# Kernel tuning notes

Measured on AMD Instinct MI355X. Metric: run time of the kernel, lower is better.

The kernel has to match this reference:

```python
import jax, jax.numpy as jnp
import numpy as np

B, L, D = 4, 2048, 1024
MD = D // 4      # memory_dim = dim // 4
K = 5            # kernel_size
DIL = 1          # dilation
EPS = 1e-6


def rmsnorm(x, w):
    return w * x * jax.lax.rsqrt(jnp.mean(x * x, axis=-1, keepdims=True) + EPS)


def setup_inputs() -> dict:
    key = jax.random.key(0)
    ks = jax.random.split(key, 16)
    n = lambda k, shape, s=0.02: jax.random.normal(k, shape, jnp.float32) * s
    return dict(
        x=jax.random.normal(ks[0], (B, L, D), jnp.float32),
        memory_state=jnp.zeros((B, MD), jnp.float32),
        norm_w=jnp.ones((D,), jnp.float32),
        dw_kernel=n(ks[1], (D, 1, K), 0.1),   # depthwise conv [O,I/g,K]
        dw_bias=jnp.zeros((D,), jnp.float32),
        pw_kernel=n(ks[2], (D, D)),           # 1x1 conv as [out,in]
        pw_bias=jnp.zeros((D,), jnp.float32),
        Win_w=n(ks[3], (MD, D)), Win_b=jnp.zeros((MD,), jnp.float32),
        Wf_w=n(ks[4], (MD, D + MD)), Wf_b=jnp.ones((MD,), jnp.float32),  # forget bias init 1.0
        Wu_w=n(ks[5], (MD, D + MD)), Wu_b=jnp.zeros((MD,), jnp.float32),
        Wo_w=n(ks[6], (D, D + MD)), Wo_b=jnp.zeros((D,), jnp.float32),
        router_w=n(ks[7], (2, D)), router_b=jnp.zeros((2,), jnp.float32),
        e0_w1=n(ks[8], (D, D)), e0_b1=jnp.zeros((D,), jnp.float32),
        e0_w2=n(ks[9], (D, D)), e0_b2=jnp.zeros((D,), jnp.float32),
        e1_w1=n(ks[10], (D, D)), e1_b1=jnp.zeros((D,), jnp.float32),
        e1_w2=n(ks[11], (D, D)), e1_b2=jnp.zeros((D,), jnp.float32),
        fnorm_w=jnp.ones((D,), jnp.float32),
        down_w=n(ks[12], (D // 4, D)), down_b=jnp.zeros((D // 4,), jnp.float32),
        up_w=n(ks[13], (D, D // 4)), up_b=jnp.zeros((D,), jnp.float32),
    )


def reference(x, memory_state, norm_w, dw_kernel, dw_bias, pw_kernel, pw_bias,
              Win_w, Win_b, Wf_w, Wf_b, Wu_w, Wu_b, Wo_w, Wo_b,
              router_w, router_b, e0_w1, e0_b1, e0_w2, e0_b2,
              e1_w1, e1_b1, e1_w2, e1_b2, fnorm_w, down_w, down_b, up_w, up_b):
    resid = x
    xn = rmsnorm(x, norm_w)                              # [B,L,D]

    # --- causal depthwise conv (left pad (K-1)*DIL == torch pad-both + slice[:L]) + pointwise ---
    P = (K - 1) * DIL
    xc = jnp.swapaxes(xn, 1, 2)                          # [B,D,L]
    xc = jax.lax.conv_general_dilated(
        xc, dw_kernel, window_strides=(1,), padding=[(P, 0)],
        rhs_dilation=(DIL,), dimension_numbers=('NCH', 'OIH', 'NCH'),
        feature_group_count=D) + dw_bias[None, :, None]
    x_conv = jnp.einsum('bdl,ed->ble', xc, pw_kernel) + pw_bias  # [B,L,D]

    # --- structured state recurrence (gated, scan over time) ---
    Wf_x, Wf_m = Wf_w[:, :D], Wf_w[:, D:]
    Wu_x, Wu_m = Wu_w[:, :D], Wu_w[:, D:]
    Wo_x, Wo_m = Wo_w[:, :D], Wo_w[:, D:]
    # precompute all x-dependent projections: [L,B,*]
    fx = jnp.einsum('bld,md->lbm', xn, Wf_x) + Wf_b
    ux = jnp.einsum('bld,md->lbm', xn, Wu_x) + Wu_b
    ox = jnp.einsum('bld,ed->lbe', xn, Wo_x) + Wo_b
    xm = jax.nn.silu(jnp.einsum('bld,md->lbm', xn, Win_w) + Win_b)
    xt = jnp.swapaxes(xn, 0, 1)                          # [L,B,D]

    def step(m, inp):
        fx_t, ux_t, ox_t, xm_t, x_t = inp
        f = jax.nn.sigmoid(fx_t + m @ Wf_m.T)
        u = jax.nn.sigmoid(ux_t + m @ Wu_m.T)
        m2 = f * m + u * xm_t
        out = x_t + ox_t + m2 @ Wo_m.T
        return m2, out

    new_mem, rec = jax.lax.scan(step, memory_state, (fx, ux, ox, xm, xt))
    x_rec = jnp.swapaxes(rec, 0, 1)                      # [B,L,D]

    y = x_conv + x_rec

    # --- enhanced gated fusion (2-expert soft MoE) ---
    r = jax.nn.softmax(y @ router_w.T + router_b, axis=-1)   # [B,L,2]
    e0 = jax.nn.silu(y @ e0_w1.T + e0_b1) @ e0_w2.T + e0_b2
    e1 = jax.nn.silu(y @ e1_w1.T + e1_b1) @ e1_w2.T + e1_b2
    y = rmsnorm(y + r[..., 0:1] * e0 + r[..., 1:2] * e1, fnorm_w)

    # --- low-rank FF (exact GELU) + residual ---
    ff = jax.nn.gelu(y @ down_w.T + down_b, approximate=False) @ up_w.T + up_b
    out = y + ff + resid
    return out, new_mem
```

## Files before the change

### kernel.cpp

```cpp
#include <hip/hip_runtime.h>
#include <hip/hip_bf16.h>

#define DD 1024
#define MDD 256
#define LL 2048
#define BB 4
#define NROWS (BB*LL)

typedef short bf16x8 __attribute__((ext_vector_type(8)));
typedef float f32x4 __attribute__((ext_vector_type(4)));
typedef int   i32x4 __attribute__((ext_vector_type(4)));

__device__ __forceinline__ short f2b(float x){
  __hip_bfloat16 h = __float2bfloat16(x);
  return *reinterpret_cast<short*>(&h);
}
__device__ __forceinline__ float b2f(short s){
  return __uint_as_float(((unsigned)(unsigned short)s) << 16);
}
__device__ __forceinline__ float frcp(float x){
#if __has_builtin(__builtin_amdgcn_rcpf)
  return __builtin_amdgcn_rcpf(x);
#else
  float r; asm("v_rcp_f32 %0, %1" : "=v"(r) : "v"(x)); return r;
#endif
}
__device__ __forceinline__ float fsigmoid(float x){
  return frcp(1.f + __expf(-x));
}
__device__ __forceinline__ float sel4(f32x4 a, int kg){
  float lo = (kg & 1) ? a[1] : a[0];
  float hi = (kg & 1) ? a[3] : a[2];
  return (kg & 2) ? hi : lo;
}

struct CvtDesc {
  const float* src; const float* src2; short* dstb; float* dstf;
  int n, cols, sld, soff, dld, mode;
};
struct CvtArgs { CvtDesc d[20]; };

__global__ __launch_bounds__(256) void cvt_all(CvtArgs a){
  int di = blockIdx.x >> 6;
  CvtDesc d = a.d[di];
  int base = (blockIdx.x & 63)*256 + threadIdx.x;
  for (int i = base; i < d.n; i += 64*256){
    int r = i / d.cols, c = i - r*d.cols;
    float v = d.src[(size_t)r*d.sld + d.soff + c];
    if (d.mode == 2) v += d.src2[i];
    if (d.mode == 0) d.dstb[(size_t)r*d.dld + c] = f2b(v);
    else             d.dstf[i] = v;
  }
}

__global__ __launch_bounds__(256) void rmsnorm_k(const float* __restrict__ x,
                                                 const float* __restrict__ w,
                                                 short* __restrict__ xn){
  int row = blockIdx.x, tid = threadIdx.x;
  const float* xr = x + (size_t)row*DD;
  float4 v = *(const float4*)&xr[tid*4];
  float ss = v.x*v.x + v.y*v.y + v.z*v.z + v.w*v.w;
  __shared__ float red[256];
  red[tid] = ss; __syncthreads();
  for (int s = 128; s > 0; s >>= 1){ if (tid < s) red[tid] += red[tid+s]; __syncthreads(); }
  float scale = rsqrtf(red[0]/(float)DD + 1e-6f);
  const float* wr = w + tid*4;
  short4 o;
  o.x = f2b(v.x*wr[0]*scale); o.y = f2b(v.y*wr[1]*scale);
  o.z = f2b(v.z*wr[2]*scale); o.w = f2b(v.w*wr[3]*scale);
  *(short4*)&xn[(size_t)row*2048 + tid*4] = o;
}

__global__ __launch_bounds__(256) void dwconv_k(const short* __restrict__ xnA,
                                                const float* __restrict__ dwk,
                                                const float* __restrict__ dwb,
                                                short* __restrict__ xcA){
  size_t i = (size_t)blockIdx.x*256 + threadIdx.x;
  int d = (int)(i & (DD-1));
  int l = (int)((i >> 10) & (LL-1));
  int b = (int)(i >> 21);
  float acc = dwb[d];
  const float* kk = dwk + d*5;
  #pragma unroll
  for (int k = 0; k < 5; ++k){
    int ll = l + k - 4;
    if (ll >= 0) acc += b2f(xnA[((size_t)(b*LL + ll))*2048 + d]) * kk[k];
  }
  xcA[((size_t)(b*LL + l))*2048 + 1024 + d] = f2b(acc);
}

template<int ACT, int OUTMODE, int PERMUTE, int DUAL>
__global__ __launch_bounds__(256) void gemm_bt(
    const short* __restrict__ A, const short* __restrict__ Bw,
    const float* __restrict__ bias, const float* __restrict__ add0,
    const float* __restrict__ add1, void* __restrict__ Cout, short* __restrict__ Cout2,
    const short* A_b, const short* Bw_b, const float* bias_b, void* Cout_b,
    int M, int N, int K, int lda, int ldb, int nbn, int nsplit){
  __shared__ __align__(16) short As[128*32];
  __shared__ __align__(16) short Bs[128*32];
  int bid = (int)blockIdx.x;
  bid = (bid & 7)*((int)gridDim.x >> 3) + (bid >> 3);
  if (DUAL && bid >= nsplit){
    A = A_b; Bw = Bw_b; bias = bias_b; Cout = Cout_b; bid -= nsplit;
  }
  int bm = bid / nbn, bn = bid % nbn;
  int tid = threadIdx.x, lane = tid & 63, w = tid >> 6;
  int wm = (w >> 1)*64, wn = (w & 1)*64;
  const int r0 = lane & 15, kg = lane >> 4;

  f32x4 acc[4][4];
  #pragma unroll
  for (int i = 0; i < 4; ++i)
    #pragma unroll
    for (int j = 0; j < 4; ++j)
      #pragma unroll
      for (int r = 0; r < 4; ++r) acc[i][j][r] = 0.f;

  const int c0 = w*64 + lane;
  const int c1 = c0 + 256;
  const short* a0 = &A [(size_t)(bm*128 + (c0 >> 2))*lda + (c0 & 3)*8];
  const short* a1 = &A [(size_t)(bm*128 + (c1 >> 2))*lda + (c1 & 3)*8];
  const short* b0 = &Bw[(size_t)(bn*128 + (c0 >> 2))*ldb + (c0 & 3)*8];
  const short* b1 = &Bw[(size_t)(bn*128 + (c1 >> 2))*ldb + (c1 & 3)*8];

  for (int k0 = 0; k0 < K; k0 += 32){
    __builtin_amdgcn_global_load_lds((const __attribute__((address_space(1))) void*)(a0 + k0),
                                     (__attribute__((address_space(3))) void*)&As[w*512], 16, 0, 0);
    __builtin_amdgcn_global_load_lds((const __attribute__((address_space(1))) void*)(b0 + k0),
                                     (__attribute__((address_space(3))) void*)&Bs[w*512], 16, 0, 0);
    __builtin_amdgcn_global_load_lds((const __attribute__((address_space(1))) void*)(a1 + k0),
                                     (__attribute__((address_space(3))) void*)&As[2048 + w*512], 16, 0, 0);
    __builtin_amdgcn_global_load_lds((const __attribute__((address_space(1))) void*)(b1 + k0),
                                     (__attribute__((address_space(3))) void*)&Bs[2048 + w*512], 16, 0, 0);
    __syncthreads();
    bf16x8 av[4], bv[4];
    #pragma unroll
    for (int i = 0; i < 4; ++i) av[i] = *(const bf16x8*)&As[(wm + i*16 + r0)*32 + kg*8];
    #pragma unroll
    for (int j = 0; j < 4; ++j) bv[j] = *(const bf16x8*)&Bs[(wn + j*16 + r0)*32 + kg*8];
    #pragma unroll
    for (int i = 0; i < 4; ++i)
      #pragma unroll
      for (int j = 0; j < 4; ++j)
        acc[i][j] = __builtin_amdgcn_mfma_f32_16x16x32_bf16(av[i], bv[j], acc[i][j], 0, 0, 0);
    __syncthreads();
  }

  #pragma unroll
  for (int i = 0; i < 4; ++i){
    int grb = bm*128 + wm + i*16 + kg*4;
    #pragma unroll
    for (int j = 0; j < 4; ++j){
      int gc = bn*128 + wn + j*16 + r0;
      float bvv = bias ? bias[gc] : 0.f;
      #pragma unroll
      for (int r = 0; r < 4; ++r){
        int gr = grb + r;
        float v = acc[i][j][r] + bvv;
        if (ACT == 1) v = v / (1.f + __expf(-v));
        else if (ACT == 2) v = 0.5f*v*(1.f + erff(v*0.70710678118f));
        size_t orow = PERMUTE ? (size_t)((gr & 3)*LL + (gr >> 2)) : (size_t)gr;
        size_t oi = orow*(size_t)N + gc;
        if (add0) v += add0[oi];
        if (add1) v += add1[oi];
        if (OUTMODE == 0) ((float*)Cout)[oi] = v;
        else if (OUTMODE == 1) ((float*)Cout)[oi] += v;
        else if (OUTMODE == 2) ((short*)Cout)[oi] = f2b(v);
        else {
          float nv = ((float*)Cout)[oi] + v;
          ((float*)Cout)[oi] = nv;
          Cout2[oi] = f2b(nv);
        }
      }
    }
  }
}

__global__ __launch_bounds__(512, 2) void scan_g34_k(
    const float* __restrict__ fxu, const short* __restrict__ Wfu,
    const float* __restrict__ m0, short* __restrict__ m2all, float* __restrict__ newmem,
    const short* __restrict__ A2, const short* __restrict__ B2,
    const float* __restrict__ bias2, const float* __restrict__ xres,
    float* __restrict__ ybuf){
  __shared__ __align__(16) short lds[8192];
  const int tid = threadIdx.x, lane = tid & 63, w = tid >> 6;
  const int r0 = lane & 15, kg = lane >> 4;

  if (blockIdx.x != 0){
    int g = (int)blockIdx.x - 1;
    g = (g & 7)*64 + (g >> 3);
    int bm = g >> 3, bn = g & 7;
    short* As = lds;
    short* Bs = lds + 4096;
    int wm = (w >> 2)*64, wn = (w & 3)*32;
    f32x4 acc[4][2];
    #pragma unroll
    for (int i = 0; i < 4; ++i)
      #pragma unroll
      for (int j = 0; j < 2; ++j)
        #pragma unroll
        for (int r = 0; r < 4; ++r) acc[i][j][r] = 0.f;

    const int c = tid;
    const short* ag = &A2[(size_t)(bm*128 + (c >> 2))*2048 + (c & 3)*8];
    const short* bg = &B2[(size_t)(bn*128 + (c >> 2))*2048 + (c & 3)*8];

    for (int k0 = 0; k0 < 2048; k0 += 32){
      __builtin_amdgcn_global_load_lds((const __attribute__((address_space(1))) void*)(ag + k0),
                                       (__attribute__((address_space(3))) void*)&As[w*512], 16, 0, 0);
      __builtin_amdgcn_global_load_lds((const __attribute__((address_space(1))) void*)(bg + k0),
                                       (__attribute__((address_space(3))) void*)&Bs[w*512], 16, 0, 0);
      __syncthreads();
      bf16x8 av[4], bv[2];
      #pragma unroll
      for (int i = 0; i < 4; ++i) av[i] = *(const bf16x8*)&As[(wm + i*16 + r0)*32 + kg*8];
      #pragma unroll
      for (int j = 0; j < 2; ++j) bv[j] = *(const bf16x8*)&Bs[(wn + j*16 + r0)*32 + kg*8];
      #pragma unroll
      for (int i = 0; i < 4; ++i)
        #pragma unroll
        for (int j = 0; j < 2; ++j)
          acc[i][j] = __builtin_amdgcn_mfma_f32_16x16x32_bf16(av[i], bv[j], acc[i][j], 0, 0, 0);
      __syncthreads();
    }
    #pragma unroll
    for (int i = 0; i < 4; ++i){
      int grb = bm*128 + wm + i*16 + kg*4;
      #pragma unroll
      for (int j = 0; j < 2; ++j){
        int gc = bn*128 + wn + j*16 + r0;
        float bvv = bias2[gc];
        #pragma unroll
        for (int r = 0; r < 4; ++r){
          size_t oi = (size_t)(grb + r)*1024 + gc;
          ybuf[oi] = acc[i][j][r] + bvv + xres[oi];
        }
      }
    }
    return;
  }

  short* mA0 = lds;
  short* mA1 = lds + 1088;
  const int j0 = w*32 + r0;

  bf16x8 bw[2][2][8];
  #pragma unroll
  for (int fu = 0; fu < 2; ++fu)
    #pragma unroll
    for (int p = 0; p < 2; ++p)
      #pragma unroll
      for (int kt = 0; kt < 8; ++kt){
        i32x4 ld = *(const i32x4*)&Wfu[(size_t)(fu*256 + w*32 + p*16 + r0)*256 + kt*32 + kg*8];
        asm volatile("" : "+v"(ld));
        bw[fu][p][kt] = __builtin_bit_cast(bf16x8, ld);
      }

  float m_reg0 = m0[kg*256 + j0];
  float m_reg1 = m0[kg*256 + j0 + 16];

  const float* pfu;
  const float* px;
  short* pm = m2all + (size_t)kg*256 + j0;
  float cf0, cf1, cu0, cu1, xmc0, xmc1, nx0, nx1;
  {
    const float* b0p = fxu + (size_t)kg*LL*768 + j0;
    cf0 = b0p[0];    cf1 = b0p[16];
    cu0 = b0p[256];  cu1 = b0p[272];
    float tx0 = b0p[512], tx1 = b0p[528];
    xmc0 = tx0*fsigmoid(tx0);  xmc1 = tx1*fsigmoid(tx1);
    nx0 = b0p[768 + 512];  nx1 = b0p[768 + 528];
    pfu = b0p + 768;
    px  = b0p + 2*768 + 512;
  }
  mA0[kg*272 + j0]      = f2b(m_reg0);
  mA0[kg*272 + j0 + 16] = f2b(m_reg1);
  __syncthreads();

  const short* mac = mA0;
  short*       man = mA1;

#define SCAN_STEP(DO_FU, DO_X)                                                         \
  {                                                                                    \
    bf16x8 af[8];                                                                      \
    _Pragma("unroll")                                                                  \
    for (int kt = 0; kt < 8; ++kt)                                                     \
      af[kt] = *(const bf16x8*)&mac[(r0 & 3)*272 + kt*32 + kg*8];                      \
    float xmn0 = nx0*fsigmoid(nx0);                                                    \
    float xmn1 = nx1*fsigmoid(nx1);                                                    \
    __builtin_amdgcn_s_setprio(1);                                                     \
    f32x4 aF0 = {0.f,0.f,0.f,0.f}, aF1 = {0.f,0.f,0.f,0.f};                            \
    f32x4 aU0 = {0.f,0.f,0.f,0.f}, aU1 = {0.f,0.f,0.f,0.f};                            \
    _Pragma("unroll")                                                                  \
    for (int kt = 0; kt < 8; ++kt){                                                    \
      aF0 = __builtin_amdgcn_mfma_f32_16x16x32_bf16(af[kt], bw[0][0][kt], aF0, 0, 0, 0); \
      aF1 = __builtin_amdgcn_mfma_f32_16x16x32_bf16(af[kt], bw[0][1][kt], aF1, 0, 0, 0); \
      aU0 = __builtin_amdgcn_mfma_f32_16x16x32_bf16(af[kt], bw[1][0][kt], aU0, 0, 0, 0); \
      aU1 = __builtin_amdgcn_mfma_f32_16x16x32_bf16(af[kt], bw[1][1][kt], aU1, 0, 0, 0); \
    }                                                                                  \
    __builtin_amdgcn_s_setprio(0);                                                     \
    float gF0 = sel4(aF0, kg), gF1 = sel4(aF1, kg);                                    \
    float gU0 = sel4(aU0, kg), gU1 = sel4(aU1, kg);                                    \
    float f0 = fsigmoid(gF0 + cf0);                                                    \
    float f1 = fsigmoid(gF1 + cf1);                                                    \
    float u0 = fsigmoid(gU0 + cu0);                                                    \
    float u1 = fsigmoid(gU1 + cu1);                                                    \
    m_reg0 = f0*m_reg0 + u0*xmc0;                                                      \
    m_reg1 = f1*m_reg1 + u1*xmc1;                                                      \
    short mb0 = f2b(m_reg0), mb1 = f2b(m_reg1);                                        \
    pm[0] = mb0; pm[16] = mb1; pm += 1024;                                             \
    xmc0 = xmn0; xmc1 = xmn1;                                                          \
    if (DO_FU){                                                                        \
      cf0 = pfu[0];    cf1 = pfu[16];                                                  \
      cu0 = pfu[256];  cu1 = pfu[272];                                                 \
      pfu += 768;                                                                      \
    }                                                                                  \
    if (DO_X){                                                                         \
      nx0 = px[0]; nx1 = px[16]; px += 768;                                            \
    }                                                                                  \
    man[kg*272 + j0]      = mb0;                                                       \
    man[kg*272 + j0 + 16] = mb1;                                                       \
    asm volatile("s_waitcnt lgkmcnt(0)" ::: "memory");                                 \
    __builtin_amdgcn_sched_barrier(0);                                                 \
    __builtin_amdgcn_s_barrier();                                                      \
    __builtin_amdgcn_sched_barrier(0);                                                 \
    { const short* tmp_ = mac; mac = man; man = (short*)tmp_; }                        \
  }

  for (int t = 0; t < LL - 2; ++t) SCAN_STEP(1, 1)
  SCAN_STEP(1, 0)
  SCAN_STEP(0, 0)
#undef SCAN_STEP

  newmem[kg*256 + j0]      = m_reg0;
  newmem[kg*256 + j0 + 16] = m_reg1;
}

__global__ __launch_bounds__(256) void combine_k(
    float* __restrict__ y, const short* __restrict__ e0, const short* __restrict__ e1,
    const float* __restrict__ rw, const float* __restrict__ rb,
    const float* __restrict__ fw, short* __restrict__ y2bf){
  int row = blockIdx.x, tid = threadIdx.x;
  size_t base = (size_t)row*DD + tid*4;
  float4 vy = *(const float4*)&y[base];
  short4 s0 = *(const short4*)&e0[base];
  short4 s1 = *(const short4*)&e1[base];
  float4 w0 = *(const float4*)&rw[tid*4];
  float4 w1 = *(const float4*)&rw[DD + tid*4];
  float d0 = vy.x*w0.x + vy.y*w0.y + vy.z*w0.z + vy.w*w0.w;
  float d1 = vy.x*w1.x + vy.y*w1.y + vy.z*w1.z + vy.w*w1.w;
  __shared__ float redA[256], redB[256];
  redA[tid] = d0; redB[tid] = d1; __syncthreads();
  for (int s = 128; s > 0; s >>= 1){
    if (tid < s){ redA[tid] += redA[tid+s]; redB[tid] += redB[tid+s]; }
    __syncthreads();
  }
  float l0 = redA[0] + rb[0], l1 = redB[0] + rb[1];
  float p0 = 1.f/(1.f + __expf(l1 - l0));
  float p1 = 1.f - p0;
  float c0 = vy.x + p0*b2f(s0.x) + p1*b2f(s1.x);
  float c1 = vy.y + p0*b2f(s0.y) + p1*b2f(s1.y);
  float c2 = vy.z + p0*b2f(s0.z) + p1*b2f(s1.z);
  float c3 = vy.w + p0*b2f(s0.w) + p1*b2f(s1.w);
  float ss = c0*c0 + c1*c1 + c2*c2 + c3*c3;
  __syncthreads();
  redA[tid] = ss; __syncthreads();
  for (int s = 128; s > 0; s >>= 1){
    if (tid < s) redA[tid] += redA[tid+s];
    __syncthreads();
  }
  float scale = rsqrtf(redA[0]/(float)DD + 1e-6f);
  const float* fwp = fw + tid*4;
  float o0 = c0*fwp[0]*scale, o1 = c1*fwp[1]*scale, o2 = c2*fwp[2]*scale, o3 = c3*fwp[3]*scale;
  float4 ov; ov.x = o0; ov.y = o1; ov.z = o2; ov.w = o3;
  *(float4*)&y[base] = ov;
  short4 ob; ob.x = f2b(o0); ob.y = f2b(o1); ob.z = f2b(o2); ob.w = f2b(o3);
  *(short4*)&y2bf[base] = ob;
}

extern "C" void kernel_launch(void* const* d_in, const int* in_sizes, int n_in,
                              void* d_out, int out_size, void* d_ws, size_t ws_size,
                              hipStream_t stream){
  (void)in_sizes; (void)n_in; (void)out_size; (void)ws_size;
  const float* x     = (const float*)d_in[0];
  const float* mem0  = (const float*)d_in[1];
  const float* normw = (const float*)d_in[2];
  const float* dwk   = (const float*)d_in[3];
  const float* dwb   = (const float*)d_in[4];
  const float* pw    = (const float*)d_in[5];
  const float* pwb   = (const float*)d_in[6];
  const float* Win_w = (const float*)d_in[7];
  const float* Win_b = (const float*)d_in[8];
  const float* Wf_w  = (const float*)d_in[9];
  const float* Wf_b  = (const float*)d_in[10];
  const float* Wu_w  = (const float*)d_in[11];
  const float* Wu_b  = (const float*)d_in[12];
  const float* Wo_w  = (const float*)d_in[13];
  const float* Wo_b  = (const float*)d_in[14];
  const float* rw    = (const float*)d_in[15];
  const float* rb    = (const float*)d_in[16];
  const float* e0w1  = (const float*)d_in[17];
  const float* e0b1  = (const float*)d_in[18];
  const float* e0w2  = (const float*)d_in[19];
  const float* e0b2  = (const float*)d_in[20];
  const float* e1w1  = (const float*)d_in[21];
  const float* e1b1  = (const float*)d_in[22];
  const float* e1w2  = (const float*)d_in[23];
  const float* e1b2  = (const float*)d_in[24];
  const float* fnw   = (const float*)d_in[25];
  const float* dnw   = (const float*)d_in[26];
  const float* dnb   = (const float*)d_in[27];
  const float* upw   = (const float*)d_in[28];
  const float* upb   = (const float*)d_in[29];

  char* ws = (char*)d_ws;
  size_t off = 0;
  auto alloc = [&](size_t bytes)->char*{
    char* p = ws + off; off += (bytes + 255) & ~(size_t)255; return p;
  };
  short* A2       = (short*)alloc((size_t)NROWS*2048*2);
  short* B2       = (short*)alloc((size_t)1024*2048*2);
  short* W_fxuwin = (short*)alloc((size_t)768*1024*2);
  short* W_fum    = (short*)alloc((size_t)512*256*2);
  short* W_om     = (short*)alloc((size_t)1024*256*2);
  short* W_e01    = (short*)alloc((size_t)2048*1024*2);
  short* W_e0w2   = (short*)alloc((size_t)1024*1024*2);
  short* W_e1w2   = (short*)alloc((size_t)1024*1024*2);
  short* W_down   = (short*)alloc((size_t)256*1024*2);
  short* W_up     = (short*)alloc((size_t)1024*256*2);
  float* bias768  = (float*)alloc(768*4);
  float* bias2    = (float*)alloc(1024*4);
  float* bias01   = (float*)alloc(2048*4);
  float* fxu      = (float*)alloc((size_t)NROWS*768*4);
  float* ybuf     = (float*)alloc((size_t)NROWS*DD*4);
  short* m2all    = (short*)alloc((size_t)NROWS*MDD*2);
  short* ybf      = (short*)alloc((size_t)NROWS*DD*2);
  short* e0v      = (short*)alloc((size_t)NROWS*DD*2);
  short* e1v      = (short*)alloc((size_t)NROWS*DD*2);
  short* h01      = (short*)alloc((size_t)NROWS*2048*2);
  short* hd = m2all;
  short* y2bf = ybf;
  float* y2   = ybuf;

  CvtArgs ca;
  auto D0 = [&](const float* s, short* db, int rows, int cols, int sld, int soff, int dld){
    return CvtDesc{s, nullptr, db, nullptr, rows*cols, cols, sld, soff, dld, 0};
  };
  auto D1 = [&](const float* s, float* df, int n){
    return CvtDesc{s, nullptr, nullptr, df, n, n, 0, 0, 0, 1};
  };
  ca.d[0]  = D0(Wo_w,  B2,                1024, 1024, 1280, 0,    2048);
  ca.d[1]  = D0(pw,    B2+1024,           1024, 1024, 1024, 0,    2048);
  ca.d[2]  = D0(Wf_w,  W_fxuwin,           256, 1024, 1280, 0,    1024);
  ca.d[3]  = D0(Wu_w,  W_fxuwin+256*1024,  256, 1024, 1280, 0,    1024);
  ca.d[4]  = D0(Win_w, W_fxuwin+512*1024,  256, 1024, 1024, 0,    1024);
  ca.d[5]  = D0(Wf_w,  W_fum,              256,  256, 1280, 1024, 256);
  ca.d[6]  = D0(Wu_w,  W_fum+256*256,      256,  256, 1280, 1024, 256);
  ca.d[7]  = D0(Wo_w,  W_om,              1024,  256, 1280, 1024, 256);
  ca.d[8]  = D0(e0w1,  W_e01,             1024, 1024, 1024, 0,    1024);
  ca.d[9]  = D0(e1w1,  W_e01+1024*1024,   1024, 1024, 1024, 0,    1024);
  ca.d[10] = D0(e0w2,  W_e0w2,            1024, 1024, 1024, 0,    1024);
  ca.d[11] = D0(e1w2,  W_e1w2,            1024, 1024, 1024, 0,    1024);
  ca.d[12] = D0(dnw,   W_down,             256, 1024, 1024, 0,    1024);
  ca.d[13] = D0(upw,   W_up,              1024,  256,  256, 0,    256);
  ca.d[14] = D1(Wf_b,  bias768,       256);
  ca.d[15] = D1(Wu_b,  bias768+256,   256);
  ca.d[16] = D1(Win_b, bias768+512,   256);
  ca.d[17] = CvtDesc{Wo_b, pwb, nullptr, bias2, 1024, 1024, 0, 0, 0, 2};
  ca.d[18] = D1(e0b1,  bias01,       1024);
  ca.d[19] = D1(e1b1,  bias01+1024,  1024);
  cvt_all<<<20*64, 256, 0, stream>>>(ca);

  rmsnorm_k<<<NROWS, 256, 0, stream>>>(x, normw, A2);
  dwconv_k<<<(NROWS*DD)/256, 256, 0, stream>>>(A2, dwk, dwb, A2);

  gemm_bt<0,0,0,0><<<64*6, 256, 0, stream>>>(A2, W_fxuwin, bias768, nullptr, nullptr,
                                             fxu, nullptr, nullptr, nullptr, nullptr, nullptr,
                                             NROWS, 768, 1024, 2048, 1024, 6, 1<<30);
  scan_g34_k<<<513, 512, 0, stream>>>(fxu, W_fum, mem0, m2all,
                                      (float*)d_out + (size_t)NROWS*DD,
                                      A2, B2, bias2, x, ybuf);
  gemm_bt<0,3,1,0><<<64*8, 256, 0, stream>>>(m2all, W_om, nullptr, nullptr, nullptr,
                                             ybuf, ybf, nullptr, nullptr, nullptr, nullptr,
                                             NROWS, 1024, 256, 256, 256, 8, 1<<30);
  gemm_bt<1,2,0,0><<<64*16, 256, 0, stream>>>(ybf, W_e01, bias01, nullptr, nullptr,
                                              h01, nullptr, nullptr, nullptr, nullptr, nullptr,
                                              NROWS, 2048, 1024, 1024, 1024, 16, 1<<30);
  gemm_bt<0,2,0,1><<<64*16, 256, 0, stream>>>(h01, W_e0w2, e0b2, nullptr, nullptr,
                                              e0v, nullptr,
                                              h01+1024, W_e1w2, e1b2, e1v,
                                              NROWS, 1024, 1024, 2048, 1024, 8, 512);
  combine_k<<<NROWS, 256, 0, stream>>>(ybuf, e0v, e1v, rw, rb, fnw, y2bf);
  gemm_bt<2,2,0,0><<<64*2, 256, 0, stream>>>(y2bf, W_down, dnb, nullptr, nullptr,
                                             hd, nullptr, nullptr, nullptr, nullptr, nullptr,
                                             NROWS, 256, 1024, 1024, 1024, 2, 1<<30);
  gemm_bt<0,0,0,0><<<64*8, 256, 0, stream>>>(hd, W_up, upb, y2, x,
                                             (float*)d_out, nullptr, nullptr, nullptr, nullptr, nullptr,
                                             NROWS, 1024, 256, 256, 256, 8, 1<<30);
}
```

Before: 1.874 ms.

## Pipeline sequential scan with downstream GEMMs in time-chunked wavefront launches

After: 2.003 ms. 1.07x slower.

```diff
diff --git a/kernel.cpp b/kernel.cpp
--- a/kernel.cpp
+++ b/kernel.cpp
@@ -6,6 +6,8 @@
 #define LL 2048
 #define BB 4
 #define NROWS (BB*LL)
+#define NCH 8
+#define TCH (LL/NCH)
 
 typedef short bf16x8 __attribute__((ext_vector_type(8)));
 typedef float f32x4 __attribute__((ext_vector_type(4)));
@@ -89,107 +91,82 @@
   xcA[((size_t)(b*LL + l))*2048 + 1024 + d] = f2b(acc);
 }
 
-template<int ACT, int OUTMODE, int PERMUTE, int DUAL>
-__global__ __launch_bounds__(256) void gemm_bt(
-    const short* __restrict__ A, const short* __restrict__ Bw,
-    const float* __restrict__ bias, const float* __restrict__ add0,
-    const float* __restrict__ add1, void* __restrict__ Cout, short* __restrict__ Cout2,
-    const short* A_b, const short* Bw_b, const float* bias_b, void* Cout_b,
-    int M, int N, int K, int lda, int ldb, int nbn, int nsplit){
-  __shared__ __align__(16) short As[128*32];
-  __shared__ __align__(16) short Bs[128*32];
-  int bid = (int)blockIdx.x;
-  bid = (bid & 7)*((int)gridDim.x >> 3) + (bid >> 3);
-  if (DUAL && bid >= nsplit){
-    A = A_b; Bw = Bw_b; bias = bias_b; Cout = Cout_b; bid -= nsplit;
-  }
-  int bm = bid / nbn, bn = bid % nbn;
-  int tid = threadIdx.x, lane = tid & 63, w = tid >> 6;
-  int wm = (w >> 1)*64, wn = (w & 1)*64;
-  const int r0 = lane & 15, kg = lane >> 4;
-
-  f32x4 acc[4][4];
-  #pragma unroll
-  for (int i = 0; i < 4; ++i)
-    #pragma unroll
-    for (int j = 0; j < 4; ++j)
-      #pragma unroll
-      for (int r = 0; r < 4; ++r) acc[i][j][r] = 0.f;
-
-  const int c0 = w*64 + lane;
-  const int c1 = c0 + 256;
-  const short* a0 = &A [(size_t)(bm*128 + (c0 >> 2))*lda + (c0 & 3)*8];
-  const short* a1 = &A [(size_t)(bm*128 + (c1 >> 2))*lda + (c1 & 3)*8];
-  const short* b0 = &Bw[(size_t)(bn*128 + (c0 >> 2))*ldb + (c0 & 3)*8];
-  const short* b1 = &Bw[(size_t)(bn*128 + (c1 >> 2))*ldb + (c1 & 3)*8];
-
-  for (int k0 = 0; k0 < K; k0 += 32){
-    __builtin_amdgcn_global_load_lds((const __attribute__((address_space(1))) void*)(a0 + k0),
-                                     (__attribute__((address_space(3))) void*)&As[w*512], 16, 0, 0);
-    __builtin_amdgcn_global_load_lds((const __attribute__((address_space(1))) void*)(b0 + k0),
-                                     (__attribute__((address_space(3))) void*)&Bs[w*512], 16, 0, 0);
-    __builtin_amdgcn_global_load_lds((const __attribute__((address_space(1))) void*)(a1 + k0),
-                                     (__attribute__((address_space(3))) void*)&As[2048 + w*512], 16, 0, 0);
-    __builtin_amdgcn_global_load_lds((const __attribute__((address_space(1))) void*)(b1 + k0),
-                                     (__attribute__((address_space(3))) void*)&Bs[2048 + w*512], 16, 0, 0);
-    __syncthreads();
-    bf16x8 av[4], bv[4];
-    #pragma unroll
-    for (int i = 0; i < 4; ++i) av[i] = *(const bf16x8*)&As[(wm + i*16 + r0)*32 + kg*8];
-    #pragma unroll
-    for (int j = 0; j < 4; ++j) bv[j] = *(const bf16x8*)&Bs[(wn + j*16 + r0)*32 + kg*8];
-    #pragma unroll
-    for (int i = 0; i < 4; ++i)
-      #pragma unroll
-      for (int j = 0; j < 4; ++j)
-        acc[i][j] = __builtin_amdgcn_mfma_f32_16x16x32_bf16(av[i], bv[j], acc[i][j], 0, 0, 0);
-    __syncthreads();
-  }
-
-  #pragma unroll
-  for (int i = 0; i < 4; ++i){
-    int grb = bm*128 + wm + i*16 + kg*4;
-    #pragma unroll
-    for (int j = 0; j < 4; ++j){
-      int gc = bn*128 + wn + j*16 + r0;
-      float bvv = bias ? bias[gc] : 0.f;
-      #pragma unroll
-      for (int r = 0; r < 4; ++r){
-        int gr = grb + r;
-        float v = acc[i][j][r] + bvv;
-        if (ACT == 1) v = v / (1.f + __expf(-v));
-        else if (ACT == 2) v = 0.5f*v*(1.f + erff(v*0.70710678118f));
-        size_t orow = PERMUTE ? (size_t)((gr & 3)*LL + (gr >> 2)) : (size_t)gr;
-        size_t oi = orow*(size_t)N + gc;
-        if (add0) v += add0[oi];
-        if (add1) v += add1[oi];
-        if (OUTMODE == 0) ((float*)Cout)[oi] = v;
-        else if (OUTMODE == 1) ((float*)Cout)[oi] += v;
-        else if (OUTMODE == 2) ((short*)Cout)[oi] = f2b(v);
-        else {
-          float nv = ((float*)Cout)[oi] + v;
-          ((float*)Cout)[oi] = nv;
-          Cout2[oi] = f2b(nv);
-        }
-      }
-    }
-  }
-}
-
-__global__ __launch_bounds__(512, 2) void scan_g34_k(
+struct Job {
+  const short* A; const short* Bw; const float* bias;
+  const float* add0; const float* add1; void* Cf; short* C2;
+  int N, K, lda, ldb, bn, nblocks, bm0, cstart, act, outmode, permute, remap, type;
+};
+struct PipeArgs { Job j[8]; int njobs; };
+
+__global__ __launch_bounds__(512, 2) void pipe_k(
     const float* __restrict__ fxu, const short* __restrict__ Wfu,
-    const float* __restrict__ m0, short* __restrict__ m2all, float* __restrict__ newmem,
-    const short* __restrict__ A2, const short* __restrict__ B2,
-    const float* __restrict__ bias2, const float* __restrict__ xres,
-    float* __restrict__ ybuf){
+    const float* __restrict__ m0, float* __restrict__ mstate,
+    short* __restrict__ m2all, float* __restrict__ newmem,
+    int t0, int nsteps, int has_scan, PipeArgs pa){
   __shared__ __align__(16) short lds[8192];
   const int tid = threadIdx.x, lane = tid & 63, w = tid >> 6;
   const int r0 = lane & 15, kg = lane >> 4;
 
-  if (blockIdx.x != 0){
-    int g = (int)blockIdx.x - 1;
-    g = (g & 7)*64 + (g >> 3);
-    int bm = g >> 3, bn = g & 7;
+  if (!has_scan || blockIdx.x != 0){
+    int jb = (int)blockIdx.x - has_scan;
+    int ji = 0;
+    while (jb >= pa.j[ji].nblocks){ jb -= pa.j[ji].nblocks; ++ji; }
+    const Job J = pa.j[ji];
+
+    if (J.type == 1){
+      float* red  = (float*)lds;
+      float* red2 = red + 512;
+      float* y = (float*)J.Cf;
+      const short* e0 = J.A; const short* e1 = J.Bw;
+      const float* rw = J.bias; const float* rb = J.add0; const float* fw = J.add1;
+      short* y2bf = J.C2;
+      int c = J.bm0;
+      float2 w0  = *(const float2*)&rw[tid*2];
+      float2 w1  = *(const float2*)&rw[1024 + tid*2];
+      float2 fw2 = *(const float2*)&fw[tid*2];
+      float rb0 = rb[0], rb1 = rb[1];
+      for (int rr = 0; rr < 4; ++rr){
+        int rl = jb*4 + rr;
+        int b = rl >> 8, t = c*256 + (rl & 255);
+        size_t base = ((size_t)b*LL + t)*1024 + tid*2;
+        float2 vy = *(const float2*)&y[base];
+        short2 s0 = *(const short2*)&e0[base];
+        short2 s1 = *(const short2*)&e1[base];
+        float d0 = vy.x*w0.x + vy.y*w0.y;
+        float d1 = vy.x*w1.x + vy.y*w1.y;
+        red[tid] = d0; red2[tid] = d1; __syncthreads();
+        for (int s = 256; s > 0; s >>= 1){
+          if (tid < s){ red[tid] += red[tid+s]; red2[tid] += red2[tid+s]; }
+          __syncthreads();
+        }
+        float l0 = red[0] + rb0, l1 = red2[0] + rb1;
+        float p0 = 1.f/(1.f + __expf(l1 - l0));
+        float p1 = 1.f - p0;
+        float c0 = vy.x + p0*b2f(s0.x) + p1*b2f(s1.x);
+        float c1 = vy.y + p0*b2f(s0.y) + p1*b2f(s1.y);
+        float ss = c0*c0 + c1*c1;
+        __syncthreads();
+        red[tid] = ss; __syncthreads();
+        for (int s = 256; s > 0; s >>= 1){
+          if (tid < s) red[tid] += red[tid+s];
+          __syncthreads();
+        }
+        float scale = rsqrtf(red[0]/1024.f + 1e-6f);
+        float o0 = c0*fw2.x*scale, o1 = c1*fw2.y*scale;
+        float2 ov; ov.x = o0; ov.y = o1;
+        *(float2*)&y[base] = ov;
+        short2 ob; ob.x = f2b(o0); ob.y = f2b(o1);
+        *(short2*)&y2bf[base] = ob;
+        __syncthreads();
+      }
+      return;
+    }
+
+    int bnidx = jb % J.bn;
+    int lb2 = jb / J.bn;
+    int bm;
+    if (J.remap == 0) bm = J.bm0 + lb2;
+    else { int c = J.cstart + (lb2 >> 3); int q = lb2 & 7; bm = (q>>1)*16 + c*2 + (q&1); }
     short* As = lds;
     short* Bs = lds + 4096;
     int wm = (w >> 2)*64, wn = (w & 3)*32;
@@ -201,11 +178,10 @@
         #pragma unroll
         for (int r = 0; r < 4; ++r) acc[i][j][r] = 0.f;
 
-    const int c = tid;
-    const short* ag = &A2[(size_t)(bm*128 + (c >> 2))*2048 + (c & 3)*8];
-    const short* bg = &B2[(size_t)(bn*128 + (c >> 2))*2048 + (c & 3)*8];
-
-    for (int k0 = 0; k0 < 2048; k0 += 32){
+    const short* ag = J.A  + (size_t)(bm*128    + (tid >> 2))*J.lda + (tid & 3)*8;
+    const short* bg = J.Bw + (size_t)(bnidx*128 + (tid >> 2))*J.ldb + (tid & 3)*8;
+
+    for (int k0 = 0; k0 < J.K; k0 += 32){
       __builtin_amdgcn_global_load_lds((const __attribute__((address_space(1))) void*)(ag + k0),
                                        (__attribute__((address_space(3))) void*)&As[w*512], 16, 0, 0);
       __builtin_amdgcn_global_load_lds((const __attribute__((address_space(1))) void*)(bg + k0),
@@ -225,15 +201,27 @@
     }
     #pragma unroll
     for (int i = 0; i < 4; ++i){
-      int grb = bm*128 + wm + i*16 + kg*4;
       #pragma unroll
       for (int j = 0; j < 2; ++j){
-        int gc = bn*128 + wn + j*16 + r0;
-        float bvv = bias2[gc];
+        int gc = bnidx*128 + wn + j*16 + r0;
+        float bvv = J.bias ? J.bias[gc] : 0.f;
         #pragma unroll
         for (int r = 0; r < 4; ++r){
-          size_t oi = (size_t)(grb + r)*1024 + gc;
-          ybuf[oi] = acc[i][j][r] + bvv + xres[oi];
+          int gr = bm*128 + wm + i*16 + kg*4 + r;
+          float v = acc[i][j][r] + bvv;
+          if (J.act == 1) v = v / (1.f + __expf(-v));
+          else if (J.act == 2) v = 0.5f*v*(1.f + erff(v*0.70710678118f));
+          size_t orow = J.permute ? (size_t)((gr & 3)*LL + (gr >> 2)) : (size_t)gr;
+          size_t oi = orow*(size_t)J.N + gc;
+          if (J.add0) v += J.add0[oi];
+          if (J.add1) v += J.add1[oi];
+          if (J.outmode == 0) ((float*)J.Cf)[oi] = v;
+          else if (J.outmode == 2) ((short*)J.Cf)[oi] = f2b(v);
+          else {
+            float nv = ((float*)J.Cf)[oi] + v;
+            ((float*)J.Cf)[oi] = nv;
+            J.C2[oi] = f2b(nv);
+          }
         }
       }
     }
@@ -256,15 +244,16 @@
         bw[fu][p][kt] = __builtin_bit_cast(bf16x8, ld);
       }
 
-  float m_reg0 = m0[kg*256 + j0];
-  float m_reg1 = m0[kg*256 + j0 + 16];
+  const float* msrc = (t0 == 0) ? m0 : mstate;
+  float m_reg0 = msrc[kg*256 + j0];
+  float m_reg1 = msrc[kg*256 + j0 + 16];
 
   const float* pfu;
   const float* px;
-  short* pm = m2all + (size_t)kg*256 + j0;
+  short* pm = m2all + (size_t)t0*1024 + kg*256 + j0;
   float cf0, cf1, cu0, cu1, xmc0, xmc1, nx0, nx1;
   {
-    const float* b0p = fxu + (size_t)kg*LL*768 + j0;
+    const float* b0p = fxu + ((size_t)kg*LL + t0)*768 + j0;
     cf0 = b0p[0];    cf1 = b0p[16];
     cu0 = b0p[256];  cu1 = b0p[272];
     float tx0 = b0p[512], tx1 = b0p[528];
@@ -327,55 +316,17 @@
     { const short* tmp_ = mac; mac = man; man = (short*)tmp_; }                        \
   }
 
-  for (int t = 0; t < LL - 2; ++t) SCAN_STEP(1, 1)
+  for (int t = 0; t < nsteps - 2; ++t) SCAN_STEP(1, 1)
   SCAN_STEP(1, 0)
   SCAN_STEP(0, 0)
 #undef SCAN_STEP
 
-  newmem[kg*256 + j0]      = m_reg0;
-  newmem[kg*256 + j0 + 16] = m_reg1;
-}
-
-__global__ __launch_bounds__(256) void combine_k(
-    float* __restrict__ y, const short* __restrict__ e0, const short* __restrict__ e1,
-    const float* __restrict__ rw, const float* __restrict__ rb,
-    const float* __restrict__ fw, short* __restrict__ y2bf){
-  int row = blockIdx.x, tid = threadIdx.x;
-  size_t base = (size_t)row*DD + tid*4;
-  float4 vy = *(const float4*)&y[base];
-  short4 s0 = *(const short4*)&e0[base];
-  short4 s1 = *(const short4*)&e1[base];
-  float4 w0 = *(const float4*)&rw[tid*4];
-  float4 w1 = *(const float4*)&rw[DD + tid*4];
-  float d0 = vy.x*w0.x + vy.y*w0.y + vy.z*w0.z + vy.w*w0.w;
-  float d1 = vy.x*w1.x + vy.y*w1.y + vy.z*w1.z + vy.w*w1.w;
-  __shared__ float redA[256], redB[256];
-  redA[tid] = d0; redB[tid] = d1; __syncthreads();
-  for (int s = 128; s > 0; s >>= 1){
-    if (tid < s){ redA[tid] += redA[tid+s]; redB[tid] += redB[tid+s]; }
-    __syncthreads();
-  }
-  float l0 = redA[0] + rb[0], l1 = redB[0] + rb[1];
-  float p0 = 1.f/(1.f + __expf(l1 - l0));
-  float p1 = 1.f - p0;
-  float c0 = vy.x + p0*b2f(s0.x) + p1*b2f(s1.x);
-  float c1 = vy.y + p0*b2f(s0.y) + p1*b2f(s1.y);
-  float c2 = vy.z + p0*b2f(s0.z) + p1*b2f(s1.z);
-  float c3 = vy.w + p0*b2f(s0.w) + p1*b2f(s1.w);
-  float ss = c0*c0 + c1*c1 + c2*c2 + c3*c3;
-  __syncthreads();
-  redA[tid] = ss; __syncthreads();
-  for (int s = 128; s > 0; s >>= 1){
-    if (tid < s) redA[tid] += redA[tid+s];
-    __syncthreads();
-  }
-  float scale = rsqrtf(redA[0]/(float)DD + 1e-6f);
-  const float* fwp = fw + tid*4;
-  float o0 = c0*fwp[0]*scale, o1 = c1*fwp[1]*scale, o2 = c2*fwp[2]*scale, o3 = c3*fwp[3]*scale;
-  float4 ov; ov.x = o0; ov.y = o1; ov.z = o2; ov.w = o3;
-  *(float4*)&y[base] = ov;
-  short4 ob; ob.x = f2b(o0); ob.y = f2b(o1); ob.z = f2b(o2); ob.w = f2b(o3);
-  *(short4*)&y2bf[base] = ob;
+  mstate[kg*256 + j0]      = m_reg0;
+  mstate[kg*256 + j0 + 16] = m_reg1;
+  if (t0 + nsteps == LL){
+    newmem[kg*256 + j0]      = m_reg0;
+    newmem[kg*256 + j0 + 16] = m_reg1;
+  }
 }
 
 extern "C" void kernel_launch(void* const* d_in, const int* in_sizes, int n_in,
@@ -431,6 +382,7 @@
   float* bias768  = (float*)alloc(768*4);
   float* bias2    = (float*)alloc(1024*4);
   float* bias01   = (float*)alloc(2048*4);
+  float* mstate   = (float*)alloc(1024*4);
   float* fxu      = (float*)alloc((size_t)NROWS*768*4);
   float* ybuf     = (float*)alloc((size_t)NROWS*DD*4);
   short* m2all    = (short*)alloc((size_t)NROWS*MDD*2);
@@ -438,9 +390,8 @@
   short* e0v      = (short*)alloc((size_t)NROWS*DD*2);
   short* e1v      = (short*)alloc((size_t)NROWS*DD*2);
   short* h01      = (short*)alloc((size_t)NROWS*2048*2);
-  short* hd = m2all;
-  short* y2bf = ybf;
-  float* y2   = ybuf;
+  short* hd       = (short*)alloc((size_t)NROWS*MDD*2);
+  float* newmem   = (float*)d_out + (size_t)NROWS*DD;
 
   CvtArgs ca;
   auto D0 = [&](const float* s, short* db, int rows, int cols, int sld, int soff, int dld){
@@ -474,27 +425,62 @@
   rmsnorm_k<<<NROWS, 256, 0, stream>>>(x, normw, A2);
   dwconv_k<<<(NROWS*DD)/256, 256, 0, stream>>>(A2, dwk, dwb, A2);
 
-  gemm_bt<0,0,0,0><<<64*6, 256, 0, stream>>>(A2, W_fxuwin, bias768, nullptr, nullptr,
-                                             fxu, nullptr, nullptr, nullptr, nullptr, nullptr,
-                                             NROWS, 768, 1024, 2048, 1024, 6, 1<<30);
-  scan_g34_k<<<513, 512, 0, stream>>>(fxu, W_fum, mem0, m2all,
-                                      (float*)d_out + (size_t)NROWS*DD,
-                                      A2, B2, bias2, x, ybuf);
-  gemm_bt<0,3,1,0><<<64*8, 256, 0, stream>>>(m2all, W_om, nullptr, nullptr, nullptr,
-                                             ybuf, ybf, nullptr, nullptr, nullptr, nullptr,
-                                             NROWS, 1024, 256, 256, 256, 8, 1<<30);
-  gemm_bt<1,2,0,0><<<64*16, 256, 0, stream>>>(ybf, W_e01, bias01, nullptr, nullptr,
-                                              h01, nullptr, nullptr, nullptr, nullptr, nullptr,
-                                              NROWS, 2048, 1024, 1024, 1024, 16, 1<<30);
-  gemm_bt<0,2,0,1><<<64*16, 256, 0, stream>>>(h01, W_e0w2, e0b2, nullptr, nullptr,
-                                              e0v, nullptr,
-                                              h01+1024, W_e1w2, e1b2, e1v,
-                                              NROWS, 1024, 1024, 2048, 1024, 8, 512);
-  combine_k<<<NROWS, 256, 0, stream>>>(ybuf, e0v, e1v, rw, rb, fnw, y2bf);
-  gemm_bt<2,2,0,0><<<64*2, 256, 0, stream>>>(y2bf, W_down, dnb, nullptr, nullptr,
-                                             hd, nullptr, nullptr, nullptr, nullptr, nullptr,
-                                             NROWS, 256, 1024, 1024, 1024, 2, 1<<30);
-  gemm_bt<0,0,0,0><<<64*8, 256, 0, stream>>>(hd, W_up, upb, y2, x,
-                                             (float*)d_out, nullptr, nullptr, nullptr, nullptr, nullptr,
-                                             NROWS, 1024, 256, 256, 256, 8, 1<<30);
-}
+  auto JG = [&](const short* A, const short* Bw, const float* bias,
+                const float* a0, const float* a1, void* Cf, short* C2,
+                int N, int K, int lda, int ldb, int bn, int nbm, int bm0, int cstart,
+                int act, int outm, int perm, int remap)->Job{
+    return Job{A, Bw, bias, a0, a1, Cf, C2, N, K, lda, ldb, bn, nbm*bn, bm0, cstart,
+               act, outm, perm, remap, 0};
+  };
+  auto G2j   = [&](int cstart, int nch)->Job{
+    return JG(A2, W_fxuwin, bias768, nullptr, nullptr, fxu, nullptr,
+              768, 1024, 2048, 1024, 6, nch*8, 0, cstart, 0, 0, 0, 1); };
+  Job G34j   = JG(A2, B2, bias2, x, nullptr, ybuf, nullptr,
+                  1024, 2048, 2048, 2048, 8, 64, 0, 0, 0, 0, 0, 0);
+  auto G5j   = [&](int k)->Job{
+    return JG(m2all, W_om, nullptr, nullptr, nullptr, ybuf, ybf,
+              1024, 256, 256, 256, 8, 8, k*8, 0, 0, 3, 1, 0); };
+  auto E1j   = [&](int k)->Job{
+    return JG(ybf, W_e01, bias01, nullptr, nullptr, h01, nullptr,
+              2048, 1024, 1024, 1024, 16, 8, 0, k, 1, 2, 0, 1); };
+  auto E2aj  = [&](int k)->Job{
+    return JG(h01, W_e0w2, e0b2, nullptr, nullptr, e0v, nullptr,
+              1024, 1024, 2048, 1024, 8, 8, 0, k, 0, 2, 0, 1); };
+  auto E2bj  = [&](int k)->Job{
+    return JG(h01+1024, W_e1w2, e1b2, nullptr, nullptr, e1v, nullptr,
+              1024, 1024, 2048, 1024, 8, 8, 0, k, 0, 2, 0, 1); };
+  auto CBj   = [&](int k)->Job{
+    return Job{(const short*)e0v, (const short*)e1v, rw, rb, fnw, ybuf, ybf,
+               0, 0, 0, 0, 0, 256, k, 0, 0, 0, 0, 0, 1}; };
+  auto G10j  = [&](int k)->Job{
+    return JG(ybf, W_down, dnb, nullptr, nullptr, hd, nullptr,
+              256, 1024, 1024, 1024, 2, 8, 0, k, 2, 2, 0, 1); };
+  auto G11j  = [&](int k)->Job{
+    return JG(hd, W_up, upb, ybuf, x, (float*)d_out, nullptr,
+              1024, 256, 256, 256, 8, 8, 0, k, 0, 0, 0, 1); };
+
+  auto launch = [&](int t0, int nsteps, std::initializer_list<Job> jobs){
+    PipeArgs pa{}; int nb = 0, nj = 0;
+    for (const Job& j : jobs){ pa.j[nj++] = j; nb += j.nblocks; }
+    pa.njobs = nj;
+    int has = nsteps > 0 ? 1 : 0;
+    pipe_k<<<has + nb, 512, 0, stream>>>(fxu, W_fum, mem0, mstate, m2all, newmem,
+                                         t0, nsteps, has, pa);
+  };
+
+  launch(0, 0, { G2j(0, 1) });
+  launch(0*TCH, TCH, { G2j(1, 7), G34j });
+  launch(1*TCH, TCH, { G5j(0) });
+  launch(2*TCH, TCH, { G5j(1), E1j(0) });
+  launch(3*TCH, TCH, { G5j(2), E1j(1), E2aj(0), E2bj(0) });
+  launch(4*TCH, TCH, { G5j(3), E1j(2), E2aj(1), E2bj(1), CBj(0) });
+  launch(5*TCH, TCH, { G5j(4), E1j(3), E2aj(2), E2bj(2), CBj(1), G10j(0) });
+  launch(6*TCH, TCH, { G5j(5), E1j(4), E2aj(3), E2bj(3), CBj(2), G10j(1), G11j(0) });
+  launch(7*TCH, TCH, { G5j(6), E1j(5), E2aj(4), E2bj(4), CBj(3), G10j(2), G11j(1) });
+  launch(0, 0, { G5j(7), E1j(6), E2aj(5), E2bj(5), CBj(4), G10j(3), G11j(2) });
+  launch(0, 0, { E1j(7), E2aj(6), E2bj(6), CBj(5), G10j(4), G11j(3) });
+  launch(0, 0, { E2aj(7), E2bj(7), CBj(6), G10j(5), G11j(4) });
+  launch(0, 0, { CBj(7), G10j(6), G11j(5) });
+  launch(0, 0, { G10j(7), G11j(6) });
+  launch(0, 0, { G11j(7) });
+}
```
